# Kernel optimization log

Hardware: AMD Instinct MI355X
Metric: run time of the kernel (lower is better)

The kernel has to match this reference:

```python
import jax, jax.numpy as jnp
import numpy as np

NEG_SLOPE = 0.2

def gatv2_layer(x, src, dst, Wl, bl, Wr, br, att, bias, N, concat):
    # Wl/Wr: [F_in, H*C]; att: [H, C]
    H, C = att.shape
    xl = (x @ Wl + bl).reshape(-1, H, C)  # source transform [N,H,C]
    xr = (x @ Wr + br).reshape(-1, H, C)  # target transform [N,H,C]
    e = jax.nn.leaky_relu(xl[src] + xr[dst], NEG_SLOPE)          # [E,H,C]
    logits = jnp.einsum('ehc,hc->eh', e, att)                    # [E,H]
    m = jax.ops.segment_max(logits, dst, num_segments=N)         # [N,H]
    p = jnp.exp(logits - m[dst])
    s = jax.ops.segment_sum(p, dst, num_segments=N)              # [N,H]
    alpha = p / s[dst]                                           # [E,H] softmax per dst
    out = jax.ops.segment_sum(alpha[:, :, None] * xl[src], dst, num_segments=N)  # [N,H,C]
    out = out.reshape(N, H * C) if concat else out.mean(axis=1)
    return out + bias


def setup_inputs() -> dict:
    key = jax.random.key(0)
    N, E, F_in = 50000, 500000, 58
    ks = jax.random.split(key, 16)
    s = 0.1
    inp = {
        'x': jax.random.normal(ks[0], (N, F_in), jnp.float32),
        'edge_index': jax.random.randint(ks[1], (2, E), 0, N, jnp.int64),
        'Wl1': jax.random.normal(ks[2], (F_in, 256), jnp.float32) * s,
        'bl1': jnp.zeros((256,), jnp.float32),
        'Wr1': jax.random.normal(ks[3], (F_in, 256), jnp.float32) * s,
        'br1': jnp.zeros((256,), jnp.float32),
        'att1': jax.random.normal(ks[4], (4, 64), jnp.float32) * s,
        'bias1': jnp.zeros((256,), jnp.float32),
        'Wl2': jax.random.normal(ks[5], (256, 256), jnp.float32) * s,
        'bl2': jnp.zeros((256,), jnp.float32),
        'Wr2': jax.random.normal(ks[6], (256, 256), jnp.float32) * s,
        'br2': jnp.zeros((256,), jnp.float32),
        'att2': jax.random.normal(ks[7], (4, 64), jnp.float32) * s,
        'bias2': jnp.zeros((256,), jnp.float32),
        'Wl3': jax.random.normal(ks[8], (256, 6), jnp.float32) * s,
        'bl3': jnp.zeros((6,), jnp.float32),
        'Wr3': jax.random.normal(ks[9], (256, 6), jnp.float32) * s,
        'br3': jnp.zeros((6,), jnp.float32),
        'att3': jax.random.normal(ks[10], (6, 1), jnp.float32) * s,
        'bias3': jnp.zeros((1,), jnp.float32),
    }
    return inp


def reference(x, edge_index, Wl1, bl1, Wr1, br1, att1, bias1,
              Wl2, bl2, Wr2, br2, att2, bias2,
              Wl3, bl3, Wr3, br3, att3, bias3):
    N = x.shape[0]
    loop = jnp.arange(N, dtype=edge_index.dtype)
    src = jnp.concatenate([edge_index[0], loop])  # self-loops (PyG default)
    dst = jnp.concatenate([edge_index[1], loop])
    h = jax.nn.elu(gatv2_layer(x, src, dst, Wl1, bl1, Wr1, br1, att1, bias1, N, True))
    h = jax.nn.elu(gatv2_layer(h, src, dst, Wl2, bl2, Wr2, br2, att2, bias2, N, True))
    out = gatv2_layer(h, src, dst, Wl3, bl3, Wr3, br3, att3, bias3, N, False)
    return out  # [N, 1]
```

## Files before the change

kernel.cpp:

```cpp
#include <hip/hip_runtime.h>
#include <math.h>

#define NEG_SLOPE 0.2f
#define LOG2E 1.4426950408889634f

typedef __attribute__((ext_vector_type(2))) _Float16 h2;
typedef __attribute__((ext_vector_type(4))) _Float16 h4;
typedef __attribute__((ext_vector_type(8))) _Float16 f16x8;
typedef __attribute__((ext_vector_type(4))) float f32x4;

template<int CTRL>
__device__ __forceinline__ float dpp_add_f32(float x) {
    int y = __builtin_amdgcn_update_dpp(0, __float_as_int(x), CTRL, 0xF, 0xF, true);
    return x + __int_as_float(y);
}
__device__ __forceinline__ float rowsum16(float x) {
    x = dpp_add_f32<0xB1>(x);
    x = dpp_add_f32<0x4E>(x);
    x = dpp_add_f32<0x124>(x);
    x = dpp_add_f32<0x128>(x);
    return x;
}


__global__ __launch_bounds__(256) void k_count(const int* __restrict__ ei, int E, int Et,
                                               int* __restrict__ cnt) {
    int e = blockIdx.x * 256 + threadIdx.x;
    if (e < Et) {
        int d = (e < E) ? ei[E + e] : (e - E);
        atomicAdd(&cnt[d], 1);
    }
}

__global__ __launch_bounds__(256) void k_scan_block(const int* __restrict__ cnt,
                                                    int* __restrict__ out,
                                                    int* __restrict__ bsums, int n) {
    __shared__ int tmp[256];
    int t = threadIdx.x;
    int i = blockIdx.x * 256 + t;
    int v = (i < n) ? cnt[i] : 0;
    tmp[t] = v;
    __syncthreads();
    for (int d = 1; d < 256; d <<= 1) {
        int add = (t >= d) ? tmp[t - d] : 0;
        __syncthreads();
        tmp[t] += add;
        __syncthreads();
    }
    if (i < n) out[i] = tmp[t] - v;
    if (t == 255) bsums[blockIdx.x] = tmp[t];
}

__global__ __launch_bounds__(256) void k_scan_bsums(int* bsums, int nb) {
    __shared__ int tmp[256];
    int t = threadIdx.x;
    int v = (t < nb) ? bsums[t] : 0;
    tmp[t] = v;
    __syncthreads();
    for (int d = 1; d < 256; d <<= 1) {
        int add = (t >= d) ? tmp[t - d] : 0;
        __syncthreads();
        tmp[t] += add;
        __syncthreads();
    }
    if (t < nb) bsums[t] = tmp[t] - v;
}

__global__ __launch_bounds__(256) void k_scan_add(int* __restrict__ out,
                                                  const int* __restrict__ bsums,
                                                  int* __restrict__ cursor,
                                                  int n, int total) {
    int i = blockIdx.x * 256 + threadIdx.x;
    if (i < n) {
        int v = out[i] + bsums[blockIdx.x];
        out[i] = v;
        cursor[i] = v;
    }
    if (i == 0) out[n] = total;
}

__global__ __launch_bounds__(256) void k_scatter(const int* __restrict__ ei, int E, int Et,
                                                 int* __restrict__ cursor,
                                                 int* __restrict__ src_sorted) {
    int e = blockIdx.x * 256 + threadIdx.x;
    if (e < Et) {
        int s, d;
        if (e < E) { s = ei[e]; d = ei[E + e]; } else { s = d = e - E; }
        int pos = atomicAdd(&cursor[d], 1);
        src_sorted[pos] = s;
    }
}


__global__ __launch_bounds__(256) void k_cast_x(const float* __restrict__ x,
                                                _Float16* __restrict__ xb,
                                                int N, int F, int kshift) {
    int i = blockIdx.x * 256 + threadIdx.x;
    if (i < (N << kshift)) {
        int n = i >> kshift, k = i & ((1 << kshift) - 1);
        float v = (k < F) ? x[n * F + k] : 0.0f;
        xb[i] = (_Float16)v;
    }
}

__global__ __launch_bounds__(256) void k_cast_w_all(
        const float* __restrict__ Wl1, const float* __restrict__ Wr1,
        const float* __restrict__ Wl2, const float* __restrict__ Wr2,
        const float* __restrict__ Wl3, const float* __restrict__ Wr3,
        _Float16* __restrict__ wtl1, _Float16* __restrict__ wtr1,
        _Float16* __restrict__ wtl2, _Float16* __restrict__ wtr2,
        _Float16* __restrict__ w3t, int F) {
    int i = blockIdx.x * 256 + threadIdx.x;
    if (i < 32768) {
        const float* W = (i < 16384) ? Wl1 : Wr1;
        _Float16* O = (i < 16384) ? wtl1 : wtr1;
        int loc = i & 16383;
        int n = loc >> 6, k = loc & 63;
        O[loc] = (_Float16)(k < F ? W[k * 256 + n] : 0.0f);
    } else if (i < 163840) {
        int seg = i - 32768;
        const float* W = (seg < 65536) ? Wl2 : Wr2;
        _Float16* O = (seg < 65536) ? wtl2 : wtr2;
        int loc = seg & 65535;
        int n = loc >> 8, k = loc & 255;
        O[loc] = (_Float16)W[k * 256 + n];
    } else if (i < 167936) {
        int loc = i - 163840;
        int j = loc >> 8, k = loc & 255;
        float v = (j < 6) ? Wl3[k * 6 + j] : ((j < 12) ? Wr3[k * 6 + (j - 6)] : 0.0f);
        w3t[loc] = (_Float16)v;
    }
}


#define LDST 40

__global__ __launch_bounds__(256, 2) void k_gemm_pair_mfma(
        const _Float16* __restrict__ A, int M, int Kp,
        const _Float16* __restrict__ Btl, const _Float16* __restrict__ Btr,
        const float* __restrict__ bl, const float* __restrict__ br,
        _Float16* __restrict__ Cl, _Float16* __restrict__ Cr) {
    __shared__ _Float16 As[128 * LDST];
    __shared__ _Float16 Bls[128 * LDST];
    __shared__ _Float16 Brs[128 * LDST];
    const int t = threadIdx.x;
    const int wave = t >> 6, lane = t & 63;
    const int wr = wave >> 1, wc = wave & 1;
    const int l15 = lane & 15, l4 = lane >> 4;
    const int row0 = blockIdx.x * 128;
    const int col0 = blockIdx.y * 128;

    f32x4 accl[4][4], accr[4][4];
    #pragma unroll
    for (int a = 0; a < 4; a++)
        #pragma unroll
        for (int b = 0; b < 4; b++) {
            accl[a][b] = (f32x4){0.f, 0.f, 0.f, 0.f};
            accr[a][b] = (f32x4){0.f, 0.f, 0.f, 0.f};
        }

    for (int k0 = 0; k0 < Kp; k0 += 32) {
        #pragma unroll
        for (int i = 0; i < 2; i++) {
            int s = t + i * 256;
            int r = s >> 2, ks = (s & 3) * 8;
            int gr = row0 + r;
            uint4 va = make_uint4(0u, 0u, 0u, 0u);
            if (gr < M) va = *(const uint4*)&A[(size_t)gr * Kp + k0 + ks];
            *(uint4*)&As[r * LDST + ks] = va;
            *(uint4*)&Bls[r * LDST + ks] = *(const uint4*)&Btl[(size_t)(col0 + r) * Kp + k0 + ks];
            *(uint4*)&Brs[r * LDST + ks] = *(const uint4*)&Btr[(size_t)(col0 + r) * Kp + k0 + ks];
        }
        __syncthreads();
        f16x8 af[4], bfl[4], bfr[4];
        #pragma unroll
        for (int mt = 0; mt < 4; mt++)
            af[mt] = *(const f16x8*)&As[(wr * 64 + mt * 16 + l15) * LDST + l4 * 8];
        #pragma unroll
        for (int nt = 0; nt < 4; nt++) {
            bfl[nt] = *(const f16x8*)&Bls[(wc * 64 + nt * 16 + l15) * LDST + l4 * 8];
            bfr[nt] = *(const f16x8*)&Brs[(wc * 64 + nt * 16 + l15) * LDST + l4 * 8];
        }
        #pragma unroll
        for (int mt = 0; mt < 4; mt++)
            #pragma unroll
            for (int nt = 0; nt < 4; nt++) {
                accl[mt][nt] = __builtin_amdgcn_mfma_f32_16x16x32_f16(
                    af[mt], bfl[nt], accl[mt][nt], 0, 0, 0);
                accr[mt][nt] = __builtin_amdgcn_mfma_f32_16x16x32_f16(
                    af[mt], bfr[nt], accr[mt][nt], 0, 0, 0);
            }
        __syncthreads();
    }
    #pragma unroll
    for (int nt = 0; nt < 4; nt++) {
        int gc = col0 + wc * 64 + nt * 16 + l15;
        float bvl = bl[gc], bvr = br[gc];
        #pragma unroll
        for (int mt = 0; mt < 4; mt++) {
            #pragma unroll
            for (int r = 0; r < 4; r++) {
                int gr = row0 + wr * 64 + mt * 16 + l4 * 4 + r;
                if (gr < M) {
                    Cl[(size_t)gr * 256 + gc] = (_Float16)(accl[mt][nt][r] + bvl);
                    Cr[(size_t)gr * 256 + gc] = (_Float16)(accr[mt][nt][r] + bvr);
                }
            }
        }
    }
}


__global__ __launch_bounds__(256) void k_gemm3_mfma(
        const _Float16* __restrict__ h,
        const _Float16* __restrict__ W3t,
        const float* __restrict__ bl, const float* __restrict__ br,
        _Float16* __restrict__ l3, int N) {
    const int wave = threadIdx.x >> 6, lane = threadIdx.x & 63;
    const int l15 = lane & 15, l4 = lane >> 4;
    const int row0 = blockIdx.x * 64 + wave * 16;
    if (row0 >= N) return;

    f16x8 bfr[8];
    #pragma unroll
    for (int ks = 0; ks < 8; ks++)
        bfr[ks] = *(const f16x8*)&W3t[l15 * 256 + ks * 32 + l4 * 8];

    const int arow = min(row0 + l15, N - 1);
    const size_t abase = (size_t)arow * 256;
    f32x4 acc = (f32x4){0.f, 0.f, 0.f, 0.f};
    #pragma unroll
    for (int ks = 0; ks < 8; ks++) {
        f16x8 af = *(const f16x8*)&h[abase + ks * 32 + l4 * 8];
        acc = __builtin_amdgcn_mfma_f32_16x16x32_f16(af, bfr[ks], acc, 0, 0, 0);
    }
    const float bv = (l15 < 6) ? bl[l15] : ((l15 < 12) ? br[l15 - 6] : 0.0f);
    #pragma unroll
    for (int r = 0; r < 4; r++) {
        int gr = row0 + l4 * 4 + r;
        if (gr < N && l15 < 12)
            l3[(size_t)gr * 16 + l15] = (_Float16)(acc[r] + bv);
    }
}


__global__ __launch_bounds__(256) void k_agg256(const _Float16* __restrict__ xl,
                                                const _Float16* __restrict__ xr,
                                                const int* __restrict__ row_ptr,
                                                const int* __restrict__ src_sorted,
                                                const float* __restrict__ att,
                                                const float* __restrict__ bias,
                                                _Float16* __restrict__ h_out, int N) {
    const int wave = threadIdx.x >> 6;
    const int lane = threadIdx.x & 63;
    const int n = __builtin_amdgcn_readfirstlane(blockIdx.x * 4 + wave);
    if (n >= N) return;
    const int ci = lane * 4;
    const h4 xr4 = *(const h4*)&xr[(size_t)n * 256 + ci];
    const float4 at4 = *(const float4*)&att[ci];
    const h2 ata = {(_Float16)(at4.x * LOG2E), (_Float16)(at4.y * LOG2E)};
    const h2 atb = {(_Float16)(at4.z * LOG2E), (_Float16)(at4.w * LOG2E)};
    float a0 = 0.f, a1 = 0.f, a2 = 0.f, a3 = 0.f;
    float m = -INFINITY, s = 0.0f;
    const int beg = row_ptr[n], end = row_ptr[n + 1];

    int j = beg;
    h4 v[8], vn[8];
    bool has = (j + 8 <= end);
    if (has) {
        #pragma unroll
        for (int e = 0; e < 8; e++) {
            int sv = src_sorted[j + e];
            v[e] = *(const h4*)&xl[(size_t)sv * 256 + ci];
        }
    }
    while (has) {
        const int jn = j + 8;
        const bool hasN = (jn + 8 <= end);
        if (hasN) {
            #pragma unroll
            for (int e = 0; e < 8; e++) {
                int sv = src_sorted[jn + e];
                vn[e] = *(const h4*)&xl[(size_t)sv * 256 + ci];
            }
        }
        float lg[8];
        #pragma unroll
        for (int e = 0; e < 8; e++) {
            h4 t = v[e] + xr4;
            h4 lk = __builtin_elementwise_max(t, t * (_Float16)NEG_SLOPE);
            h2 lo = __builtin_shufflevector(lk, lk, 0, 1);
            h2 hi = __builtin_shufflevector(lk, lk, 2, 3);
            lg[e] = __builtin_amdgcn_fdot2(lo, ata,
                        __builtin_amdgcn_fdot2(hi, atb, 0.0f, false), false);
        }
        #pragma unroll
        for (int e = 0; e < 8; e++) lg[e] = rowsum16(lg[e]);
        float bm = fmaxf(fmaxf(fmaxf(lg[0], lg[1]), fmaxf(lg[2], lg[3])),
                         fmaxf(fmaxf(lg[4], lg[5]), fmaxf(lg[6], lg[7])));
        float nm = fmaxf(m, bm);
        float sc = __builtin_amdgcn_exp2f(m - nm);
        a0 *= sc; a1 *= sc; a2 *= sc; a3 *= sc;
        float ps = 0.f;
        #pragma unroll
        for (int e = 0; e < 8; e++) {
            float p = __builtin_amdgcn_exp2f(lg[e] - nm);
            ps += p;
            a0 = fmaf(p, (float)v[e].x, a0);
            a1 = fmaf(p, (float)v[e].y, a1);
            a2 = fmaf(p, (float)v[e].z, a2);
            a3 = fmaf(p, (float)v[e].w, a3);
        }
        s = s * sc + ps;
        m = nm;
        if (hasN) {
            #pragma unroll
            for (int e = 0; e < 8; e++) v[e] = vn[e];
        }
        j = jn;
        has = hasN;
    }
    for (; j < end; j++) {
        int sv = src_sorted[j];
        h4 vv = *(const h4*)&xl[(size_t)sv * 256 + ci];
        h4 t = vv + xr4;
        h4 lk = __builtin_elementwise_max(t, t * (_Float16)NEG_SLOPE);
        h2 lo = __builtin_shufflevector(lk, lk, 0, 1);
        h2 hi = __builtin_shufflevector(lk, lk, 2, 3);
        float lg = __builtin_amdgcn_fdot2(lo, ata,
                       __builtin_amdgcn_fdot2(hi, atb, 0.0f, false), false);
        lg = rowsum16(lg);
        float nm = fmaxf(m, lg);
        float sc = __builtin_amdgcn_exp2f(m - nm);
        float p  = __builtin_amdgcn_exp2f(lg - nm);
        a0 = fmaf(p, (float)vv.x, a0 * sc);
        a1 = fmaf(p, (float)vv.y, a1 * sc);
        a2 = fmaf(p, (float)vv.z, a2 * sc);
        a3 = fmaf(p, (float)vv.w, a3 * sc);
        s = s * sc + p;
        m = nm;
    }
    const float inv = 1.0f / s;
    const float4 bv = *(const float4*)&bias[ci];
    float o0 = a0 * inv + bv.x;
    float o1 = a1 * inv + bv.y;
    float o2 = a2 * inv + bv.z;
    float o3 = a3 * inv + bv.w;
    o0 = o0 > 0.f ? o0 : (__expf(o0) - 1.f);
    o1 = o1 > 0.f ? o1 : (__expf(o1) - 1.f);
    o2 = o2 > 0.f ? o2 : (__expf(o2) - 1.f);
    o3 = o3 > 0.f ? o3 : (__expf(o3) - 1.f);
    h4 hv = {(_Float16)o0, (_Float16)o1, (_Float16)o2, (_Float16)o3};
    *(h4*)&h_out[(size_t)n * 256 + ci] = hv;
}


__global__ __launch_bounds__(64) void k_agg3(const _Float16* __restrict__ l3,
                                             const int* __restrict__ row_ptr,
                                             const int* __restrict__ src_sorted,
                                             const float* __restrict__ att3,
                                             const float* __restrict__ bias3,
                                             float* __restrict__ out, int N) {
    int n = blockIdx.x * 64 + threadIdx.x;
    if (n >= N) return;
    const h4* pn = (const h4*)&l3[(size_t)n * 16];
    h4 q1 = pn[1], q2 = pn[2];
    float xrv[6];
    xrv[0] = (float)q1.z; xrv[1] = (float)q1.w;
    xrv[2] = (float)q2.x; xrv[3] = (float)q2.y;
    xrv[4] = (float)q2.z; xrv[5] = (float)q2.w;
    float attv[6], m[6], s[6], acc[6];
    #pragma unroll
    for (int k = 0; k < 6; k++) {
        attv[k] = att3[k] * LOG2E;
        m[k] = -INFINITY; s[k] = 0.0f; acc[k] = 0.0f;
    }
    int beg = row_ptr[n], end = row_ptr[n + 1];
    for (int idx = beg; idx < end; idx++) {
        int sv = src_sorted[idx];
        const h4* ps = (const h4*)&l3[(size_t)sv * 16];
        h4 u0 = ps[0], u1 = ps[1];
        float xlv[6];
        xlv[0] = (float)u0.x; xlv[1] = (float)u0.y;
        xlv[2] = (float)u0.z; xlv[3] = (float)u0.w;
        xlv[4] = (float)u1.x; xlv[5] = (float)u1.y;
        #pragma unroll
        for (int k = 0; k < 6; k++) {
            float tt = xlv[k] + xrv[k];
            float lr = fmaxf(tt, NEG_SLOPE * tt);
            float logit = attv[k] * lr;
            float nm = fmaxf(m[k], logit);
            float sc = __builtin_amdgcn_exp2f(m[k] - nm);
            float p  = __builtin_amdgcn_exp2f(logit - nm);
            acc[k] = acc[k] * sc + p * xlv[k];
            s[k]   = s[k] * sc + p;
            m[k]   = nm;
        }
    }
    float o = 0.0f;
    #pragma unroll
    for (int k = 0; k < 6; k++) o += acc[k] / s[k];
    out[n] = o * (1.0f / 6.0f) + bias3[0];
}


extern "C" void kernel_launch(void* const* d_in, const int* in_sizes, int n_in,
                              void* d_out, int out_size, void* d_ws, size_t ws_size,
                              hipStream_t stream) {
    const float* x    = (const float*)d_in[0];
    const int*   ei   = (const int*)  d_in[1];
    const float* Wl1  = (const float*)d_in[2];
    const float* bl1  = (const float*)d_in[3];
    const float* Wr1  = (const float*)d_in[4];
    const float* br1  = (const float*)d_in[5];
    const float* att1 = (const float*)d_in[6];
    const float* bias1= (const float*)d_in[7];
    const float* Wl2  = (const float*)d_in[8];
    const float* bl2  = (const float*)d_in[9];
    const float* Wr2  = (const float*)d_in[10];
    const float* br2  = (const float*)d_in[11];
    const float* att2 = (const float*)d_in[12];
    const float* bias2= (const float*)d_in[13];
    const float* Wl3  = (const float*)d_in[14];
    const float* bl3  = (const float*)d_in[15];
    const float* Wr3  = (const float*)d_in[16];
    const float* br3  = (const float*)d_in[17];
    const float* att3 = (const float*)d_in[18];
    const float* bias3= (const float*)d_in[19];

    const int F  = in_sizes[2] / 256;
    const int N  = in_sizes[0] / F;
    const int E  = in_sizes[1] / 2;
    const int Et = E + N;

    char* ws = (char*)d_ws;
    size_t off = 0;
    auto carve = [&](size_t bytes) -> char* {
        char* p = ws + off;
        off = (off + bytes + 255) & ~(size_t)255;
        return p;
    };
    _Float16* xb   = (_Float16*)carve((size_t)N * 64 * 2);
    _Float16* xlb  = (_Float16*)carve((size_t)N * 256 * 2);
    _Float16* xrb  = (_Float16*)carve((size_t)N * 256 * 2);
    _Float16* hb   = (_Float16*)carve((size_t)N * 256 * 2);
    _Float16* wtl1 = (_Float16*)carve(256 * 64 * 2);
    _Float16* wtr1 = (_Float16*)carve(256 * 64 * 2);
    _Float16* wtl2 = (_Float16*)carve(256 * 256 * 2);
    _Float16* wtr2 = (_Float16*)carve(256 * 256 * 2);
    _Float16* w3t  = (_Float16*)carve(16 * 256 * 2);
    _Float16* l3   = (_Float16*)carve((size_t)N * 16 * 2);
    int* cnt        = (int*)carve((size_t)N * 4);
    int* row_ptr    = (int*)carve((size_t)(N + 1) * 4);
    int* cursor     = (int*)carve((size_t)N * 4);
    int* src_sorted = (int*)carve((size_t)Et * 4);
    int* bsums      = (int*)carve(1024 * 4);

    const int gN  = (N + 255) / 256;
    const int gEt = (Et + 255) / 256;
    const int gW  = (N + 3) / 4;

    hipMemsetAsync(cnt, 0, (size_t)N * 4, stream);
    k_count<<<gEt, 256, 0, stream>>>(ei, E, Et, cnt);
    k_scan_block<<<gN, 256, 0, stream>>>(cnt, row_ptr, bsums, N);
    k_scan_bsums<<<1, 256, 0, stream>>>(bsums, gN);
    k_scan_add<<<gN, 256, 0, stream>>>(row_ptr, bsums, cursor, N, Et);
    k_scatter<<<gEt, 256, 0, stream>>>(ei, E, Et, cursor, src_sorted);

    k_cast_x<<<((N << 6) + 255) / 256, 256, 0, stream>>>(x, xb, N, F, 6);
    k_cast_w_all<<<656, 256, 0, stream>>>(Wl1, Wr1, Wl2, Wr2, Wl3, Wr3,
                                          wtl1, wtr1, wtl2, wtr2, w3t, F);

    dim3 gemm_grid((N + 127) / 128, 2);

    k_gemm_pair_mfma<<<gemm_grid, 256, 0, stream>>>(xb, N, 64, wtl1, wtr1, bl1, br1, xlb, xrb);
    k_agg256<<<gW, 256, 0, stream>>>(xlb, xrb, row_ptr, src_sorted, att1, bias1, hb, N);

    k_gemm_pair_mfma<<<gemm_grid, 256, 0, stream>>>(hb, N, 256, wtl2, wtr2, bl2, br2, xlb, xrb);
    k_agg256<<<gW, 256, 0, stream>>>(xlb, xrb, row_ptr, src_sorted, att2, bias2, hb, N);

    k_gemm3_mfma<<<(N + 63) / 64, 256, 0, stream>>>(hb, w3t, bl3, br3, l3, N);
    k_agg3<<<(N + 63) / 64, 64, 0, stream>>>(l3, row_ptr, src_sorted, att3, bias3,
                                             (float*)d_out, N);
}
```

Measured before the change: 353.9 us.

## Rewrite paired GEMM to load MFMA fragments directly from global memory

The paired Wl/Wr GEMM drops its LDS staging and block-wide barriers. Each wave now loads f16 fragments straight from global memory and computes a 64x64 tile for one of the two matrices. The block tile shrinks from 128 to 64 rows. Operands are swapped (weights as A, activations as B) so each lane holds four consecutive output columns and can store an h4 vector with bias added. This removes LDS traffic and syncs, but row data is no longer shared across waves and must be re-read through cache, and the loads are strided rather than coalesced.

```diff
diff --git a/kernel.cpp b/kernel.cpp
--- a/kernel.cpp
+++ b/kernel.cpp
@@ -133,78 +133,64 @@
 }
 
 
-#define LDST 40
-
-__global__ __launch_bounds__(256, 2) void k_gemm_pair_mfma(
+__global__ __launch_bounds__(256) void k_gemm_pair_mfma(
         const _Float16* __restrict__ A, int M, int Kp,
         const _Float16* __restrict__ Btl, const _Float16* __restrict__ Btr,
         const float* __restrict__ bl, const float* __restrict__ br,
         _Float16* __restrict__ Cl, _Float16* __restrict__ Cr) {
-    __shared__ _Float16 As[128 * LDST];
-    __shared__ _Float16 Bls[128 * LDST];
-    __shared__ _Float16 Brs[128 * LDST];
-    const int t = threadIdx.x;
-    const int wave = t >> 6, lane = t & 63;
-    const int wr = wave >> 1, wc = wave & 1;
+    const int wave = threadIdx.x >> 6, lane = threadIdx.x & 63;
     const int l15 = lane & 15, l4 = lane >> 4;
-    const int row0 = blockIdx.x * 128;
-    const int col0 = blockIdx.y * 128;
-
-    f32x4 accl[4][4], accr[4][4];
+    const int row0 = blockIdx.x * 64;
+    const int mat  = wave >> 1;
+    const int col0 = blockIdx.y * 128 + (wave & 1) * 64;
+    const _Float16* Bt = mat ? Btr : Btl;
+    const float* bias  = mat ? br  : bl;
+    _Float16* C        = mat ? Cr  : Cl;
+
+    f32x4 acc[4][4];
     #pragma unroll
     for (int a = 0; a < 4; a++)
         #pragma unroll
-        for (int b = 0; b < 4; b++) {
-            accl[a][b] = (f32x4){0.f, 0.f, 0.f, 0.f};
-            accr[a][b] = (f32x4){0.f, 0.f, 0.f, 0.f};
-        }
+        for (int b = 0; b < 4; b++)
+            acc[a][b] = (f32x4){0.f, 0.f, 0.f, 0.f};
+
+    int xrow[4];
+    #pragma unroll
+    for (int nt = 0; nt < 4; nt++) xrow[nt] = min(row0 + nt * 16 + l15, M - 1);
+    const _Float16* wbase = Bt + (size_t)(col0 + l15) * Kp + l4 * 8;
+    const _Float16* xbase = A + l4 * 8;
 
     for (int k0 = 0; k0 < Kp; k0 += 32) {
-        #pragma unroll
-        for (int i = 0; i < 2; i++) {
-            int s = t + i * 256;
-            int r = s >> 2, ks = (s & 3) * 8;
-            int gr = row0 + r;
-            uint4 va = make_uint4(0u, 0u, 0u, 0u);
-            if (gr < M) va = *(const uint4*)&A[(size_t)gr * Kp + k0 + ks];
-            *(uint4*)&As[r * LDST + ks] = va;
-            *(uint4*)&Bls[r * LDST + ks] = *(const uint4*)&Btl[(size_t)(col0 + r) * Kp + k0 + ks];
-            *(uint4*)&Brs[r * LDST + ks] = *(const uint4*)&Btr[(size_t)(col0 + r) * Kp + k0 + ks];
-        }
-        __syncthreads();
-        f16x8 af[4], bfl[4], bfr[4];
-        #pragma unroll
-        for (int mt = 0; mt < 4; mt++)
-            af[mt] = *(const f16x8*)&As[(wr * 64 + mt * 16 + l15) * LDST + l4 * 8];
-        #pragma unroll
-        for (int nt = 0; nt < 4; nt++) {
-            bfl[nt] = *(const f16x8*)&Bls[(wc * 64 + nt * 16 + l15) * LDST + l4 * 8];
-            bfr[nt] = *(const f16x8*)&Brs[(wc * 64 + nt * 16 + l15) * LDST + l4 * 8];
-        }
-        #pragma unroll
-        for (int mt = 0; mt < 4; mt++)
+        f16x8 wf[4], xf[4];
+        #pragma unroll
+        for (int ct = 0; ct < 4; ct++)
+            wf[ct] = *(const f16x8*)(wbase + (size_t)(ct * 16) * Kp + k0);
+        #pragma unroll
+        for (int nt = 0; nt < 4; nt++)
+            xf[nt] = *(const f16x8*)(xbase + (size_t)xrow[nt] * Kp + k0);
+        #pragma unroll
+        for (int ct = 0; ct < 4; ct++)
             #pragma unroll
-            for (int nt = 0; nt < 4; nt++) {
-                accl[mt][nt] = __builtin_amdgcn_mfma_f32_16x16x32_f16(
-                    af[mt], bfl[nt], accl[mt][nt], 0, 0, 0);
-                accr[mt][nt] = __builtin_amdgcn_mfma_f32_16x16x32_f16(
-                    af[mt], bfr[nt], accr[mt][nt], 0, 0, 0);
-            }
-        __syncthreads();
-    }
+            for (int nt = 0; nt < 4; nt++)
+                acc[ct][nt] = __builtin_amdgcn_mfma_f32_16x16x32_f16(
+                    wf[ct], xf[nt], acc[ct][nt], 0, 0, 0);
+    }
+
+    float4 bv[4];
+    #pragma unroll
+    for (int ct = 0; ct < 4; ct++)
+        bv[ct] = *(const float4*)&bias[col0 + ct * 16 + l4 * 4];
     #pragma unroll
     for (int nt = 0; nt < 4; nt++) {
-        int gc = col0 + wc * 64 + nt * 16 + l15;
-        float bvl = bl[gc], bvr = br[gc];
-        #pragma unroll
-        for (int mt = 0; mt < 4; mt++) {
+        int node = row0 + nt * 16 + l15;
+        if (node < M) {
             #pragma unroll
-            for (int r = 0; r < 4; r++) {
-                int gr = row0 + wr * 64 + mt * 16 + l4 * 4 + r;
-                if (gr < M) {
-                    Cl[(size_t)gr * 256 + gc] = (_Float16)(accl[mt][nt][r] + bvl);
-                    Cr[(size_t)gr * 256 + gc] = (_Float16)(accr[mt][nt][r] + bvr);
-                }
+            for (int ct = 0; ct < 4; ct++) {
+                h4 hv = {(_Float16)(acc[ct][nt][0] + bv[ct].x),
+                         (_Float16)(acc[ct][nt][1] + bv[ct].y),
+                         (_Float16)(acc[ct][nt][2] + bv[ct].z),
+                         (_Float16)(acc[ct][nt][3] + bv[ct].w)};
+                *(h4*)&C[(size_t)node * 256 + col0 + ct * 16 + l4 * 4] = hv;
             }
         }
     }
@@ -471,7 +457,7 @@
     k_cast_w_all<<<656, 256, 0, stream>>>(Wl1, Wr1, Wl2, Wr2, Wl3, Wr3,
                                           wtl1, wtr1, wtl2, wtr2, w3t, F);
 
-    dim3 gemm_grid((N + 127) / 128, 2);
+    dim3 gemm_grid((N + 63) / 64, 2);
 
     k_gemm_pair_mfma<<<gemm_grid, 256, 0, stream>>>(xb, N, 64, wtl1, wtr1, bl1, br1, xlb, xrb);
     k_agg256<<<gW, 256, 0, stream>>>(xlb, xrb, row_ptr, src_sorted, att1, bias1, hb, N);
```

Result: slower. 363.8 us (+2.8%).
